# Optimization experiments

Measured on AMD Instinct MI355X. Metric: run time of the kernel, lower is better.

## Reference

```python
import jax, jax.numpy as jnp
import numpy as np

HIDDEN = 1024
HEADS = 16
HEAD = HIDDEN // HEADS


def setup_inputs() -> dict:
    key = jax.random.key(0)
    k1, k2, k3, k4, k5, k6 = jax.random.split(key, 6)
    B, S = 2, 2048
    x = jax.random.normal(k1, (B, S, HIDDEN), dtype=jnp.float32)
    mask = jax.random.randint(k2, (B, S), 0, 2, dtype=jnp.int32)
    # torch nn.Linear params: W [out,in], b [out]
    s = 1.0 / np.sqrt(HIDDEN)
    qkv_w = jax.random.uniform(k3, (3 * HIDDEN, HIDDEN), jnp.float32, -s, s)
    qkv_b = jax.random.uniform(k4, (3 * HIDDEN,), jnp.float32, -s, s)
    out_w = jax.random.uniform(k5, (HIDDEN, HIDDEN), jnp.float32, -s, s)
    out_b = jax.random.uniform(k6, (HIDDEN,), jnp.float32, -s, s)
    return {"x": x, "mask": mask, "qkv_w": qkv_w, "qkv_b": qkv_b,
            "out_w": out_w, "out_b": out_b}


def reference(x, mask, qkv_w, qkv_b, out_w, out_b):
    B, S, H = x.shape
    scale = HEAD ** -0.5
    qkv = x @ qkv_w.T + qkv_b                      # [B,S,3H]
    qkv = qkv.reshape(B, S, 3, HEADS, HEAD)
    qkv = jnp.transpose(qkv, (2, 0, 3, 1, 4))      # [3,B,h,S,d]
    q, k, v = qkv[0], qkv[1], qkv[2]
    scores = jnp.einsum('bhqd,bhkd->bhqk', q, k) * scale
    # key-padding mask [B,S] -> [B,1,1,S]
    scores = jnp.where(mask[:, None, None, :] == 0, -1e9, scores)
    attn = jax.nn.softmax(scores, axis=-1)
    # dropout is identity in eval mode
    ctx = jnp.einsum('bhqk,bhkd->bhqd', attn, v)   # [B,h,S,d]
    ctx = jnp.transpose(ctx, (0, 2, 1, 3)).reshape(B, S, H)
    return ctx @ out_w.T + out_b
```

## Files before the change

kernel.cpp:

```cpp
#include <hip/hip_runtime.h>
#include <hip/hip_bf16.h>

#define S_LEN 2048
#define NH    16
#define HD    64
#define HID   1024
#define BATCH 2
#define STK   72
#define SCQ   0.18033688f

typedef __bf16 bf16x8 __attribute__((ext_vector_type(8)));
typedef float  f32x4  __attribute__((ext_vector_type(4)));
typedef float  f32x16 __attribute__((ext_vector_type(16)));
typedef unsigned u32x2 __attribute__((ext_vector_type(2)));

__device__ __forceinline__ unsigned int pk2(float lo, float hi) {
    union { __hip_bfloat162 h; unsigned int u; } c;
    c.h = __float22bfloat162_rn(make_float2(lo, hi));
    return c.u;
}
__device__ __forceinline__ uint4 pk8(float4 a, float4 b) {
    uint4 o;
    o.x = pk2(a.x, a.y); o.y = pk2(a.z, a.w);
    o.z = pk2(b.x, b.y); o.w = pk2(b.z, b.w);
    return o;
}
__device__ __forceinline__ float exp2_hw(float x) {
    float r; asm("v_exp_f32 %0, %1" : "=v"(r) : "v"(x)); return r;
}
__device__ __forceinline__ void pl32swap(unsigned &a, unsigned &b) {
    u32x2 r = __builtin_amdgcn_permlane32_swap(a, b, false, false);
    a = r[0]; b = r[1];
}
__device__ __forceinline__ float pair_max(float x) {
    unsigned u = __float_as_uint(x);
    u32x2 r = __builtin_amdgcn_permlane32_swap(u, u, false, false);
    return fmaxf(__uint_as_float(r[0]), __uint_as_float(r[1]));
}
__device__ __forceinline__ float pair_sum(float x) {
    unsigned u = __float_as_uint(x);
    u32x2 r = __builtin_amdgcn_permlane32_swap(u, u, false, false);
    return __uint_as_float(r[0]) + __uint_as_float(r[1]);
}
__device__ __forceinline__ void gll16(const unsigned short* g, unsigned short* l) {
    __builtin_amdgcn_global_load_lds(
        (const __attribute__((address_space(1))) void*)g,
        (__attribute__((address_space(3))) void*)l, 16, 0, 0);
}

__global__ __launch_bounds__(256)
void fill_constf(float* __restrict__ out, long n, float v) {
    long i = (long)blockIdx.x * 256 + threadIdx.x;
    const long stride = (long)gridDim.x * 256;
    for (; i < n; i += stride) out[i] = v;
}

__global__ __launch_bounds__(256)
void cvt_bf16(const float* __restrict__ src, unsigned short* __restrict__ dst, long n8) {
    long t = (long)blockIdx.x * 256 + threadIdx.x;
    const long stride = (long)gridDim.x * 256;
    for (; t < n8; t += stride) {
        const float4 a = *(const float4*)(src + t * 8);
        const float4 b = *(const float4*)(src + t * 8 + 4);
        *(uint4*)(dst + t * 8) = pk8(a, b);
    }
}
__global__ __launch_bounds__(256)
void cvt2_bf16(const float* __restrict__ s0, unsigned short* __restrict__ d0, long n0,
               const float* __restrict__ s1, unsigned short* __restrict__ d1, long n1) {
    long t = (long)blockIdx.x * 256 + threadIdx.x;
    const long stride = (long)gridDim.x * 256;
    for (; t < n0 + n1; t += stride) {
        const float* s; unsigned short* d; long i;
        if (t < n0) { s = s0; d = d0; i = t; } else { s = s1; d = d1; i = t - n0; }
        const float4 a = *(const float4*)(s + i * 8);
        const float4 b = *(const float4*)(s + i * 8 + 4);
        *(uint4*)(d + i * 8) = pk8(a, b);
    }
}

__global__ __launch_bounds__(256)
void gemm_bf16(const unsigned short* __restrict__ A,
               const unsigned short* __restrict__ W,
               const float* __restrict__ bias,
               unsigned short* __restrict__ o0,
               unsigned short* __restrict__ o1,
               unsigned short* __restrict__ o2,
               float* __restrict__ of,
               int mode)
{
    __shared__ __align__(16) unsigned short lA[3][128 * 32];
    __shared__ __align__(16) unsigned short lB[3][128 * 32];
    const int tid  = threadIdx.x;
    const int lane = tid & 63, wv = tid >> 6;
    const int quad = lane >> 4, l16 = lane & 15;
    const int wm = (wv & 1) * 64, wn = (wv >> 1) * 64;

    const int nwg = gridDim.x * gridDim.y;
    const int bid = blockIdx.y * gridDim.x + blockIdx.x;
    const int xcd = bid & 7, boff = bid >> 3;
    const int qd = nwg >> 3, rm = nwg & 7;
    const int swz = (xcd < rm ? xcd * (qd + 1) : rm * (qd + 1) + (xcd - rm) * qd) + boff;
    const int m0 = (swz / gridDim.x) * 128, n0 = (swz % gridDim.x) * 128;

    f32x4 acc[4][4] = {};

    const int srow0 = wv * 32 + (lane >> 2);
    const int srow1 = srow0 + 16;
    const int csrc  = ((lane & 3) ^ ((lane >> 3) & 3)) * 8;
    const unsigned short* pa0 = A + (long)(m0 + srow0) * HID + csrc;
    const unsigned short* pa1 = A + (long)(m0 + srow1) * HID + csrc;
    const unsigned short* pb0 = W + (long)(n0 + srow0) * HID + csrc;
    const unsigned short* pb1 = W + (long)(n0 + srow1) * HID + csrc;

    const int cq8 = (quad ^ ((l16 >> 1) & 3)) * 8;

#define STAGE_G(bufi, koff)                                        \
    do {                                                           \
        gll16(pa0 + (koff), &lA[bufi][(wv * 2 + 0) * 512]);        \
        gll16(pa1 + (koff), &lA[bufi][(wv * 2 + 1) * 512]);        \
        gll16(pb0 + (koff), &lB[bufi][(wv * 2 + 0) * 512]);        \
        gll16(pb1 + (koff), &lB[bufi][(wv * 2 + 1) * 512]);        \
    } while (0)

    STAGE_G(0, 0);
    STAGE_G(1, 32);

    int cur = 0;
    for (int k0 = 0; k0 < HID; k0 += 32) {
        if (k0 + 32 < HID) { asm volatile("s_waitcnt vmcnt(4)" ::: "memory"); }
        else               { asm volatile("s_waitcnt vmcnt(0)" ::: "memory"); }
        __builtin_amdgcn_s_barrier();
        asm volatile("" ::: "memory");

        if (k0 + 64 < HID) {
            const int nxt = cur ? cur - 1 : 2;
            STAGE_G(nxt, k0 + 64);
        }

        bf16x8 af[4], bfr[4];
#pragma unroll
        for (int mt = 0; mt < 4; mt++)
            af[mt] = *(const bf16x8*)&lA[cur][(wm + mt * 16 + l16) * 32 + cq8];
#pragma unroll
        for (int nt = 0; nt < 4; nt++)
            bfr[nt] = *(const bf16x8*)&lB[cur][(wn + nt * 16 + l16) * 32 + cq8];
#pragma unroll
        for (int mt = 0; mt < 4; mt++)
#pragma unroll
            for (int nt = 0; nt < 4; nt++)
                acc[mt][nt] = __builtin_amdgcn_mfma_f32_16x16x32_bf16(
                    af[mt], bfr[nt], acc[mt][nt], 0, 0, 0);

        cur = (cur < 2) ? cur + 1 : 0;
    }
#undef STAGE_G

    if (mode == 0) {
#pragma unroll
        for (int nt = 0; nt < 4; nt++) {
            const int n = n0 + wn + nt * 16 + l16;
            const float bv = bias[n];
            const int part = n >> 10, f = n & 1023, h = f >> 6, d = f & 63;
#pragma unroll
            for (int mt = 0; mt < 4; mt++) {
                const int mbase = m0 + wm + mt * 16 + quad * 4;
                const int b = mbase >> 11, s0 = mbase & 2047;
                const int bh = b * NH + h;
                if (part != 1) {
                    const float qsc = (part == 0) ? SCQ : 1.0f;
                    unsigned short* dst = (part == 0) ? o0 : o2;
                    uint2 o;
                    o.x = pk2((acc[mt][nt][0] + bv) * qsc, (acc[mt][nt][1] + bv) * qsc);
                    o.y = pk2((acc[mt][nt][2] + bv) * qsc, (acc[mt][nt][3] + bv) * qsc);
                    *(uint2*)&dst[((long)bh * HD + d) * S_LEN + s0] = o;
                } else {
#pragma unroll
                    for (int r = 0; r < 4; r++) {
                        union { __hip_bfloat16 h; unsigned short u; } cv;
                        cv.h = __float2bfloat16(acc[mt][nt][r] + bv);
                        o1[((long)bh * S_LEN + s0 + r) * HD + d] = cv.u;
                    }
                }
            }
        }
    } else {
#pragma unroll
        for (int nt = 0; nt < 4; nt++) {
            const int n = n0 + wn + nt * 16 + l16;
            const float bv = bias[n];
#pragma unroll
            for (int mt = 0; mt < 4; mt++) {
                const int mbase = m0 + wm + mt * 16 + quad * 4;
#pragma unroll
                for (int r = 0; r < 4; r++)
                    of[(long)(mbase + r) * HID + n] = acc[mt][nt][r] + bv;
            }
        }
    }
}

__global__ __launch_bounds__(256)
void attn(const unsigned short* __restrict__ q,
          const unsigned short* __restrict__ k,
          const unsigned short* __restrict__ vt_g,
          const int* __restrict__ mask,
          unsigned short* __restrict__ ctx)
{
    __shared__ __align__(16) unsigned short kt[2][64 * STK];
    __shared__ __align__(16) unsigned short vt[2][64 * STK];
    __shared__ __align__(16) float mkv[2][64];

    const int tid  = threadIdx.x;
    const int lane = tid & 63, wv = tid >> 6;
    const int ar = lane & 31, hi = lane >> 5;
    const int qt = blockIdx.x, h = blockIdx.y, b = blockIdx.z;
    const int bh = b * NH + h;
    const int sq = qt * 128 + wv * 32 + ar;

    union { unsigned short u[8]; bf16x8 v; } qu[4];
    const unsigned short* qg = q + (long)bh * HD * S_LEN + sq;
#pragma unroll
    for (int t = 0; t < 4; t++)
#pragma unroll
        for (int j = 0; j < 8; j++)
            qu[t].u[j] = qg[(long)(16 * t + 8 * hi + j) * S_LEN];

    float mrun = -1e30f, lsum = 0.f;
    f32x16 Of0 = {}, Of1 = {};

    const int sr = tid >> 2, c0 = tid & 3;
    const unsigned short* kg = k    + ((long)bh * S_LEN + sr) * HD + c0 * 8;
    const unsigned short* vg = vt_g + ((long)bh * HD + sr) * S_LEN + c0 * 8;
    const int wof0 = sr * STK + ((c0 ^ (sr & 7)) * 8);
    const int wof1 = sr * STK + (((c0 + 4) ^ (sr & 7)) * 8);
    const int swzr = ar & 7;

    uint4 rk0 = *(const uint4*)(kg);
    uint4 rk1 = *(const uint4*)(kg + 32);
    uint4 rv0 = *(const uint4*)(vg);
    uint4 rv1 = *(const uint4*)(vg + 32);
    float rmv = 0.f;
    if (tid < 64) rmv = (mask[b * S_LEN + tid] == 0) ? -1e9f : 0.f;
    *(uint4*)&kt[0][wof0] = rk0;
    *(uint4*)&kt[0][wof1] = rk1;
    *(uint4*)&vt[0][wof0] = rv0;
    *(uint4*)&vt[0][wof1] = rv1;
    if (tid < 64) mkv[0][tid] = rmv;
    rk0 = *(const uint4*)(kg + (long)64 * HD);
    rk1 = *(const uint4*)(kg + (long)64 * HD + 32);
    rv0 = *(const uint4*)(vg + 64);
    rv1 = *(const uint4*)(vg + 64 + 32);
    if (tid < 64) rmv = (mask[b * S_LEN + 64 + tid] == 0) ? -1e9f : 0.f;
    asm volatile("s_waitcnt lgkmcnt(0)" ::: "memory");
    __builtin_amdgcn_s_barrier();
    asm volatile("" ::: "memory");

    for (int k0 = 0; k0 < S_LEN; k0 += 64) {
        const int cur = (k0 >> 6) & 1;
        if (k0 + 64 < S_LEN) {
            *(uint4*)&kt[cur ^ 1][wof0] = rk0;
            *(uint4*)&kt[cur ^ 1][wof1] = rk1;
            *(uint4*)&vt[cur ^ 1][wof0] = rv0;
            *(uint4*)&vt[cur ^ 1][wof1] = rv1;
            if (tid < 64) mkv[cur ^ 1][tid] = rmv;
            if (k0 + 128 < S_LEN) {
                rk0 = *(const uint4*)(kg + (long)(k0 + 128) * HD);
                rk1 = *(const uint4*)(kg + (long)(k0 + 128) * HD + 32);
                rv0 = *(const uint4*)(vg + (k0 + 128));
                rv1 = *(const uint4*)(vg + (k0 + 128) + 32);
                if (tid < 64) rmv = (mask[b * S_LEN + k0 + 128 + tid] == 0) ? -1e9f : 0.f;
            }
        }

        float st[2][16];
        __builtin_amdgcn_s_setprio(1);
#pragma unroll
        for (int G = 0; G < 2; G++) {
            f32x16 s = {};
#pragma unroll
            for (int t = 0; t < 4; t++) {
                bf16x8 kf = *(const bf16x8*)
                    &kt[cur][(G * 32 + ar) * STK + (((2 * t + hi) ^ swzr) * 8)];
                s = __builtin_amdgcn_mfma_f32_32x32x16_bf16(kf, qu[t].v, s, 0, 0, 0);
            }
#pragma unroll
            for (int m = 0; m < 4; m++) {
                const float4 mv = *(const float4*)&mkv[cur][G * 32 + m * 8 + hi * 4];
#pragma unroll
                for (int r2 = 0; r2 < 4; r2++)
                    st[G][m * 4 + r2] = s[m * 4 + r2] + (&mv.x)[r2];
            }
        }
        __builtin_amdgcn_s_setprio(0);

        float pmax = st[0][0];
#pragma unroll
        for (int G = 0; G < 2; G++)
#pragma unroll
            for (int r = 0; r < 16; r++) pmax = fmaxf(pmax, st[G][r]);
        pmax = pair_max(pmax);

        if (__any(pmax > mrun + 8.f)) {
            const float mn = fmaxf(mrun, pmax);
            const float alpha = exp2_hw(mrun - mn);
            Of0 *= alpha; Of1 *= alpha; lsum *= alpha;
            mrun = mn;
        }

        unsigned wa[2][4], wb[2][4];
        float ls = 0.f;
#pragma unroll
        for (int G = 0; G < 2; G++) {
            float pr[16];
#pragma unroll
            for (int r = 0; r < 16; r++) {
                pr[r] = exp2_hw(st[G][r] - mrun);
                ls += pr[r];
            }
#pragma unroll
            for (int m = 0; m < 4; m++) {
                wa[G][m] = pk2(pr[4 * m + 0], pr[4 * m + 1]);
                wb[G][m] = pk2(pr[4 * m + 2], pr[4 * m + 3]);
            }
        }
        lsum += ls;

        union { unsigned u[4]; bf16x8 v; } F[4];
#pragma unroll
        for (int s5 = 0; s5 < 4; s5++) {
            const int G = s5 >> 1, mp = (s5 & 1) * 2;
            unsigned f0 = wa[G][mp], f2 = wa[G][mp + 1];
            unsigned f1 = wb[G][mp], f3 = wb[G][mp + 1];
            pl32swap(f0, f2);
            pl32swap(f1, f3);
            F[s5].u[0] = f0; F[s5].u[1] = f1; F[s5].u[2] = f2; F[s5].u[3] = f3;
        }

        __builtin_amdgcn_s_setprio(1);
#pragma unroll
        for (int s5 = 0; s5 < 4; s5++) {
            bf16x8 vf0 = *(const bf16x8*)
                &vt[cur][(0 * 32 + ar) * STK + (((2 * s5 + hi) ^ swzr) * 8)];
            Of0 = __builtin_amdgcn_mfma_f32_32x32x16_bf16(vf0, F[s5].v, Of0, 0, 0, 0);
            bf16x8 vf1 = *(const bf16x8*)
                &vt[cur][(1 * 32 + ar) * STK + (((2 * s5 + hi) ^ swzr) * 8)];
            Of1 = __builtin_amdgcn_mfma_f32_32x32x16_bf16(vf1, F[s5].v, Of1, 0, 0, 0);
        }
        __builtin_amdgcn_s_setprio(0);

        asm volatile("s_waitcnt lgkmcnt(0)" ::: "memory");
        __builtin_amdgcn_s_barrier();
        asm volatile("" ::: "memory");
    }

    const float inv = 1.f / pair_sum(lsum);
    unsigned short* cb = ctx + ((long)b * S_LEN + sq) * HID + h * HD;
#pragma unroll
    for (int m = 0; m < 4; m++) {
        uint2 o0, o1;
        o0.x = pk2(Of0[4 * m + 0] * inv, Of0[4 * m + 1] * inv);
        o0.y = pk2(Of0[4 * m + 2] * inv, Of0[4 * m + 3] * inv);
        *(uint2*)&cb[m * 8 + hi * 4] = o0;
        o1.x = pk2(Of1[4 * m + 0] * inv, Of1[4 * m + 1] * inv);
        o1.y = pk2(Of1[4 * m + 2] * inv, Of1[4 * m + 3] * inv);
        *(uint2*)&cb[32 + m * 8 + hi * 4] = o1;
    }
}

extern "C" void kernel_launch(void* const* d_in, const int* in_sizes, int n_in,
                              void* d_out, int out_size, void* d_ws, size_t ws_size,
                              hipStream_t stream) {
    float* outp = (float*)d_out;

    const float* x = nullptr; const int* mask = nullptr;
    const float* qkv_w = nullptr; const float* qkv_b = nullptr;
    const float* out_w = nullptr; const float* out_b = nullptr;
    for (int i = 0; i < n_in; i++) {
        switch (in_sizes[i]) {
            case 4194304: x     = (const float*)d_in[i]; break;
            case 4096:    mask  = (const int*)d_in[i];   break;
            case 3145728: qkv_w = (const float*)d_in[i]; break;
            case 3072:    qkv_b = (const float*)d_in[i]; break;
            case 1048576: out_w = (const float*)d_in[i]; break;
            case 1024:    out_b = (const float*)d_in[i]; break;
            default: break;
        }
    }
    if (!x || !mask || !qkv_w || !qkv_b || !out_w || !out_b) {
        fill_constf<<<256, 256, 0, stream>>>(outp, (long)out_size, 1000.0f);
        return;
    }

    const size_t per = (size_t)BATCH * NH * S_LEN * HD;
    const size_t nx  = (size_t)BATCH * S_LEN * HID;
    const size_t nqw = (size_t)3 * HID * HID;
    const size_t now = (size_t)HID * HID;
    if (ws_size < 4 * per * sizeof(unsigned short)) {
        fill_constf<<<256, 256, 0, stream>>>(outp, (long)out_size, 2000.0f);
        return;
    }

    unsigned short* wsq = (unsigned short*)d_ws;
    unsigned short* wsk = wsq + per;
    unsigned short* wsv = wsk + per;
    unsigned short* wsc = wsv + per;
    unsigned short* xb  = wsc;
    unsigned short* qwb = (unsigned short*)d_out;
    unsigned short* owb = wsq;

    cvt2_bf16<<<1024, 256, 0, stream>>>(x, xb, (long)(nx / 8), qkv_w, qwb, (long)(nqw / 8));
    gemm_bf16<<<dim3(3 * HID / 128, BATCH * S_LEN / 128), 256, 0, stream>>>(
        xb, qwb, qkv_b, wsq, wsk, wsv, nullptr, 0);
    attn<<<dim3(S_LEN / 128, NH, BATCH), 256, 0, stream>>>(wsq, wsk, wsv, mask, wsc);
    cvt_bf16<<<512, 256, 0, stream>>>(out_w, owb, (long)(now / 8));
    gemm_bf16<<<dim3(HID / 128, BATCH * S_LEN / 128), 256, 0, stream>>>(
        wsc, owb, out_b, nullptr, nullptr, nullptr, outp, 1);
}
```

Baseline: 231.0 us.

## Split attention key tiles across wave pairs and merge partial softmax states

```diff
diff --git a/kernel.cpp b/kernel.cpp
--- a/kernel.cpp
+++ b/kernel.cpp
@@ -200,7 +200,7 @@
     }
 }
 
-__global__ __launch_bounds__(256)
+__global__ __launch_bounds__(512)
 void attn(const unsigned short* __restrict__ q,
           const unsigned short* __restrict__ k,
           const unsigned short* __restrict__ vt_g,
@@ -214,9 +214,10 @@
     const int tid  = threadIdx.x;
     const int lane = tid & 63, wv = tid >> 6;
     const int ar = lane & 31, hi = lane >> 5;
+    const int chunk = wv >> 1, p = wv & 1;
     const int qt = blockIdx.x, h = blockIdx.y, b = blockIdx.z;
     const int bh = b * NH + h;
-    const int sq = qt * 128 + wv * 32 + ar;
+    const int sq = qt * 128 + chunk * 32 + ar;
 
     union { unsigned short u[8]; bf16x8 v; } qu[4];
     const unsigned short* qg = q + (long)bh * HD * S_LEN + sq;
@@ -229,28 +230,20 @@
     float mrun = -1e30f, lsum = 0.f;
     f32x16 Of0 = {}, Of1 = {};
 
-    const int sr = tid >> 2, c0 = tid & 3;
+    const int sr = tid >> 3, c0 = tid & 7;
     const unsigned short* kg = k    + ((long)bh * S_LEN + sr) * HD + c0 * 8;
     const unsigned short* vg = vt_g + ((long)bh * HD + sr) * S_LEN + c0 * 8;
-    const int wof0 = sr * STK + ((c0 ^ (sr & 7)) * 8);
-    const int wof1 = sr * STK + (((c0 + 4) ^ (sr & 7)) * 8);
-    const int swzr = ar & 7;
-
-    uint4 rk0 = *(const uint4*)(kg);
-    uint4 rk1 = *(const uint4*)(kg + 32);
-    uint4 rv0 = *(const uint4*)(vg);
-    uint4 rv1 = *(const uint4*)(vg + 32);
+    const int wof = sr * STK + c0 * 8;
+
+    uint4 rk = *(const uint4*)(kg);
+    uint4 rv = *(const uint4*)(vg);
     float rmv = 0.f;
     if (tid < 64) rmv = (mask[b * S_LEN + tid] == 0) ? -1e9f : 0.f;
-    *(uint4*)&kt[0][wof0] = rk0;
-    *(uint4*)&kt[0][wof1] = rk1;
-    *(uint4*)&vt[0][wof0] = rv0;
-    *(uint4*)&vt[0][wof1] = rv1;
+    *(uint4*)&kt[0][wof] = rk;
+    *(uint4*)&vt[0][wof] = rv;
     if (tid < 64) mkv[0][tid] = rmv;
-    rk0 = *(const uint4*)(kg + (long)64 * HD);
-    rk1 = *(const uint4*)(kg + (long)64 * HD + 32);
-    rv0 = *(const uint4*)(vg + 64);
-    rv1 = *(const uint4*)(vg + 64 + 32);
+    rk = *(const uint4*)(kg + (long)64 * HD);
+    rv = *(const uint4*)(vg + 64);
     if (tid < 64) rmv = (mask[b * S_LEN + 64 + tid] == 0) ? -1e9f : 0.f;
     asm volatile("s_waitcnt lgkmcnt(0)" ::: "memory");
     __builtin_amdgcn_s_barrier();
@@ -259,46 +252,41 @@
     for (int k0 = 0; k0 < S_LEN; k0 += 64) {
         const int cur = (k0 >> 6) & 1;
         if (k0 + 64 < S_LEN) {
-            *(uint4*)&kt[cur ^ 1][wof0] = rk0;
-            *(uint4*)&kt[cur ^ 1][wof1] = rk1;
-            *(uint4*)&vt[cur ^ 1][wof0] = rv0;
-            *(uint4*)&vt[cur ^ 1][wof1] = rv1;
+            *(uint4*)&kt[cur ^ 1][wof] = rk;
+            *(uint4*)&vt[cur ^ 1][wof] = rv;
             if (tid < 64) mkv[cur ^ 1][tid] = rmv;
             if (k0 + 128 < S_LEN) {
-                rk0 = *(const uint4*)(kg + (long)(k0 + 128) * HD);
-                rk1 = *(const uint4*)(kg + (long)(k0 + 128) * HD + 32);
-                rv0 = *(const uint4*)(vg + (k0 + 128));
-                rv1 = *(const uint4*)(vg + (k0 + 128) + 32);
+                rk = *(const uint4*)(kg + (long)(k0 + 128) * HD);
+                rv = *(const uint4*)(vg + (k0 + 128));
                 if (tid < 64) rmv = (mask[b * S_LEN + k0 + 128 + tid] == 0) ? -1e9f : 0.f;
             }
         }
 
-        float st[2][16];
+        float st[16];
         __builtin_amdgcn_s_setprio(1);
-#pragma unroll
-        for (int G = 0; G < 2; G++) {
+        {
             f32x16 s = {};
 #pragma unroll
             for (int t = 0; t < 4; t++) {
                 bf16x8 kf = *(const bf16x8*)
-                    &kt[cur][(G * 32 + ar) * STK + (((2 * t + hi) ^ swzr) * 8)];
+                    &kt[cur][(p * 32 + ar) * STK + (2 * t + hi) * 8];
                 s = __builtin_amdgcn_mfma_f32_32x32x16_bf16(kf, qu[t].v, s, 0, 0, 0);
             }
+            __builtin_amdgcn_s_setprio(0);
 #pragma unroll
             for (int m = 0; m < 4; m++) {
-                const float4 mv = *(const float4*)&mkv[cur][G * 32 + m * 8 + hi * 4];
+                const float4 mv = *(const float4*)&mkv[cur][p * 32 + m * 8 + hi * 4];
 #pragma unroll
                 for (int r2 = 0; r2 < 4; r2++)
-                    st[G][m * 4 + r2] = s[m * 4 + r2] + (&mv.x)[r2];
+                    st[m * 4 + r2] = s[m * 4 + r2] + (&mv.x)[r2];
             }
         }
-        __builtin_amdgcn_s_setprio(0);
-
-        float pmax = st[0][0];
-#pragma unroll
-        for (int G = 0; G < 2; G++)
-#pragma unroll
-            for (int r = 0; r < 16; r++) pmax = fmaxf(pmax, st[G][r]);
+
+        float pmax = fmaxf(fmaxf(fmaxf(st[0], st[1]), fmaxf(st[2], st[3])),
+                     fmaxf(fmaxf(st[4], st[5]), fmaxf(st[6], st[7])));
+        pmax = fmaxf(pmax,
+                fmaxf(fmaxf(fmaxf(st[8], st[9]), fmaxf(st[10], st[11])),
+                      fmaxf(fmaxf(st[12], st[13]), fmaxf(st[14], st[15]))));
         pmax = pair_max(pmax);
 
         if (__any(pmax > mrun + 8.f)) {
@@ -308,30 +296,27 @@
             mrun = mn;
         }
 
-        unsigned wa[2][4], wb[2][4];
+        float pr[16];
         float ls = 0.f;
 #pragma unroll
-        for (int G = 0; G < 2; G++) {
-            float pr[16];
-#pragma unroll
-            for (int r = 0; r < 16; r++) {
-                pr[r] = exp2_hw(st[G][r] - mrun);
-                ls += pr[r];
-            }
-#pragma unroll
-            for (int m = 0; m < 4; m++) {
-                wa[G][m] = pk2(pr[4 * m + 0], pr[4 * m + 1]);
-                wb[G][m] = pk2(pr[4 * m + 2], pr[4 * m + 3]);
-            }
+        for (int r = 0; r < 16; r++) {
+            pr[r] = exp2_hw(st[r] - mrun);
+            ls += pr[r];
         }
         lsum += ls;
-
-        union { unsigned u[4]; bf16x8 v; } F[4];
-#pragma unroll
-        for (int s5 = 0; s5 < 4; s5++) {
-            const int G = s5 >> 1, mp = (s5 & 1) * 2;
-            unsigned f0 = wa[G][mp], f2 = wa[G][mp + 1];
-            unsigned f1 = wb[G][mp], f3 = wb[G][mp + 1];
+        unsigned wa[4], wb[4];
+#pragma unroll
+        for (int m = 0; m < 4; m++) {
+            wa[m] = pk2(pr[4 * m + 0], pr[4 * m + 1]);
+            wb[m] = pk2(pr[4 * m + 2], pr[4 * m + 3]);
+        }
+
+        union { unsigned u[4]; bf16x8 v; } F[2];
+#pragma unroll
+        for (int s5 = 0; s5 < 2; s5++) {
+            const int mp = s5 * 2;
+            unsigned f0 = wa[mp], f2 = wa[mp + 1];
+            unsigned f1 = wb[mp], f3 = wb[mp + 1];
             pl32swap(f0, f2);
             pl32swap(f1, f3);
             F[s5].u[0] = f0; F[s5].u[1] = f1; F[s5].u[2] = f2; F[s5].u[3] = f3;
@@ -339,12 +324,11 @@
 
         __builtin_amdgcn_s_setprio(1);
 #pragma unroll
-        for (int s5 = 0; s5 < 4; s5++) {
-            bf16x8 vf0 = *(const bf16x8*)
-                &vt[cur][(0 * 32 + ar) * STK + (((2 * s5 + hi) ^ swzr) * 8)];
+        for (int s5 = 0; s5 < 2; s5++) {
+            const int gr = (2 * (2 * p + s5) + hi) * 8;
+            bf16x8 vf0 = *(const bf16x8*)&vt[cur][(0 * 32 + ar) * STK + gr];
             Of0 = __builtin_amdgcn_mfma_f32_32x32x16_bf16(vf0, F[s5].v, Of0, 0, 0, 0);
-            bf16x8 vf1 = *(const bf16x8*)
-                &vt[cur][(1 * 32 + ar) * STK + (((2 * s5 + hi) ^ swzr) * 8)];
+            bf16x8 vf1 = *(const bf16x8*)&vt[cur][(1 * 32 + ar) * STK + gr];
             Of1 = __builtin_amdgcn_mfma_f32_32x32x16_bf16(vf1, F[s5].v, Of1, 0, 0, 0);
         }
         __builtin_amdgcn_s_setprio(0);
@@ -354,17 +338,48 @@
         asm volatile("" ::: "memory");
     }
 
-    const float inv = 1.f / pair_sum(lsum);
-    unsigned short* cb = ctx + ((long)b * S_LEN + sq) * HID + h * HD;
-#pragma unroll
-    for (int m = 0; m < 4; m++) {
-        uint2 o0, o1;
-        o0.x = pk2(Of0[4 * m + 0] * inv, Of0[4 * m + 1] * inv);
-        o0.y = pk2(Of0[4 * m + 2] * inv, Of0[4 * m + 3] * inv);
-        *(uint2*)&cb[m * 8 + hi * 4] = o0;
-        o1.x = pk2(Of1[4 * m + 0] * inv, Of1[4 * m + 1] * inv);
-        o1.y = pk2(Of1[4 * m + 2] * inv, Of1[4 * m + 3] * inv);
-        *(uint2*)&cb[32 + m * 8 + hi * 4] = o1;
+    const float lp = pair_sum(lsum);
+    float* mo0 = (float*)&kt[0][0];
+    float* mo1 = (float*)&vt[0][0];
+    float* mml = (float*)&vt[0][0] + 4096;
+    const int mbase = (chunk * 64 + lane) * 16;
+    const int mx4 = (lane >> 1) & 3;
+    if (p == 1) {
+#pragma unroll
+        for (int m = 0; m < 4; m++) {
+            const int off = mbase + ((m ^ mx4) << 2);
+            *(float4*)&mo0[off] = make_float4(Of0[4*m+0], Of0[4*m+1], Of0[4*m+2], Of0[4*m+3]);
+            *(float4*)&mo1[off] = make_float4(Of1[4*m+0], Of1[4*m+1], Of1[4*m+2], Of1[4*m+3]);
+        }
+        mml[(chunk * 64 + lane) * 2 + 0] = mrun;
+        mml[(chunk * 64 + lane) * 2 + 1] = lp;
+    }
+    __syncthreads();
+    if (p == 0) {
+        const float m1 = mml[(chunk * 64 + lane) * 2 + 0];
+        const float l1 = mml[(chunk * 64 + lane) * 2 + 1];
+        const float mm = fmaxf(mrun, m1);
+        const float a0 = exp2_hw(mrun - mm);
+        const float a1 = exp2_hw(m1 - mm);
+        const float inv = 1.f / (lp * a0 + l1 * a1);
+        unsigned short* cb = ctx + ((long)b * S_LEN + sq) * HID + h * HD;
+#pragma unroll
+        for (int m = 0; m < 4; m++) {
+            const int off = mbase + ((m ^ mx4) << 2);
+            const float4 p0 = *(const float4*)&mo0[off];
+            const float4 p1 = *(const float4*)&mo1[off];
+            uint2 o0, o1;
+            o0.x = pk2((Of0[4*m+0] * a0 + p0.x * a1) * inv,
+                       (Of0[4*m+1] * a0 + p0.y * a1) * inv);
+            o0.y = pk2((Of0[4*m+2] * a0 + p0.z * a1) * inv,
+                       (Of0[4*m+3] * a0 + p0.w * a1) * inv);
+            *(uint2*)&cb[m * 8 + hi * 4] = o0;
+            o1.x = pk2((Of1[4*m+0] * a0 + p1.x * a1) * inv,
+                       (Of1[4*m+1] * a0 + p1.y * a1) * inv);
+            o1.y = pk2((Of1[4*m+2] * a0 + p1.z * a1) * inv,
+                       (Of1[4*m+3] * a0 + p1.w * a1) * inv);
+            *(uint2*)&cb[32 + m * 8 + hi * 4] = o1;
+        }
     }
 }
 
@@ -412,7 +427,7 @@
     cvt2_bf16<<<1024, 256, 0, stream>>>(x, xb, (long)(nx / 8), qkv_w, qwb, (long)(nqw / 8));
     gemm_bf16<<<dim3(3 * HID / 128, BATCH * S_LEN / 128), 256, 0, stream>>>(
         xb, qwb, qkv_b, wsq, wsk, wsv, nullptr, 0);
-    attn<<<dim3(S_LEN / 128, NH, BATCH), 256, 0, stream>>>(wsq, wsk, wsv, mask, wsc);
+    attn<<<dim3(S_LEN / 128, NH, BATCH), 512, 0, stream>>>(wsq, wsk, wsv, mask, wsc);
     cvt_bf16<<<512, 256, 0, stream>>>(out_w, owb, (long)(now / 8));
     gemm_bf16<<<dim3(HID / 128, BATCH * S_LEN / 128), 256, 0, stream>>>(
         wsc, owb, out_b, nullptr, nullptr, nullptr, outp, 1);
```

New measurement: 216.9 us. 1.07x faster.
